# Kernel tuning notes

Hardware: AMD Instinct MI355X
Metric: run time of the kernel (lower is better)

The kernel has to match this reference:

```python
import jax, jax.numpy as jnp
import numpy as np
import math

B, S, D, H = 4, 1024, 1024, 16
DK = D // H
DF = 4 * D
SPARSITY = 0.3
EPS = 1e-5

def _ln(x, g, b):
    mu = jnp.mean(x, axis=-1, keepdims=True)
    var = jnp.mean((x - mu) ** 2, axis=-1, keepdims=True)
    return (x - mu) * jax.lax.rsqrt(var + EPS) * g + b

def setup_inputs() -> dict:
    key = jax.random.key(0)
    ks = jax.random.split(key, 8)
    sc = 0.02
    return {
        "x": jax.random.normal(ks[0], (B, S, D), jnp.float32),
        "Wq": jax.random.normal(ks[1], (D, D), jnp.float32) * sc,
        "bq": jnp.zeros((D,), jnp.float32),
        "Wk": jax.random.normal(ks[2], (D, D), jnp.float32) * sc,
        "bk": jnp.zeros((D,), jnp.float32),
        "Wv": jax.random.normal(ks[3], (D, D), jnp.float32) * sc,
        "bv": jnp.zeros((D,), jnp.float32),
        "Wo": jax.random.normal(ks[4], (D, D), jnp.float32) * sc,
        "bo": jnp.zeros((D,), jnp.float32),
        "W1": jax.random.normal(ks[5], (DF, D), jnp.float32) * sc,
        "b1": jnp.zeros((DF,), jnp.float32),
        "Wm": jax.random.normal(ks[6], (DF, DF), jnp.float32) * sc,
        "bm": jnp.zeros((DF,), jnp.float32),
        "W2": jax.random.normal(ks[7], (D, DF), jnp.float32) * sc,
        "b2": jnp.zeros((D,), jnp.float32),
        "g1": jnp.ones((D,), jnp.float32),
        "be1": jnp.zeros((D,), jnp.float32),
        "g2": jnp.ones((D,), jnp.float32),
        "be2": jnp.zeros((D,), jnp.float32),
    }

def reference(x, Wq, bq, Wk, bk, Wv, bv, Wo, bo, W1, b1, Wm, bm, W2, b2, g1, be1, g2, be2):
    h = _ln(x, g1, be1)
    def heads(W, b):
        return (h @ W.T + b).reshape(B, S, H, DK).transpose(0, 2, 1, 3)  # [B,H,S,DK]
    Q, K, V = heads(Wq, bq), heads(Wk, bk), heads(Wv, bv)
    scores = jnp.einsum("bhqd,bhkd->bhqk", Q, K) / math.sqrt(DK)  # [B,H,S,S]
    k = max(1, int(S * SPARSITY))
    vals, idx = jax.lax.top_k(scores, k)  # [B,H,S,k]
    # scatter top-k values into a -inf canvas (faithful to torch scatter_)
    N = B * H * S
    rows = jnp.arange(N)[:, None]
    mask2 = jnp.full((N, S), -jnp.inf, scores.dtype)
    mask2 = mask2.at[rows, idx.reshape(N, k)].set(vals.reshape(N, k))
    attn = jax.nn.softmax(mask2.reshape(B, H, S, S), axis=-1)
    out = jnp.einsum("bhqk,bhkd->bhqd", attn, V)
    out = out.transpose(0, 2, 1, 3).reshape(B, S, D) @ Wo.T + bo
    x = x + out
    h2 = _ln(x, g2, be2)
    f = jax.nn.gelu(h2 @ W1.T + b1, approximate=False)
    f = jax.nn.gelu(f @ Wm.T + bm, approximate=False)
    f = f @ W2.T + b2
    x = x + f
    return x, attn
```

## Files before the change

### kernel.cpp

```cpp
#include <hip/hip_runtime.h>
#include <hip/hip_bf16.h>

typedef __hip_bfloat16 bf16;
typedef float v4f __attribute__((ext_vector_type(4)));
typedef short v8s __attribute__((ext_vector_type(8)));

#define KSEL 307

__device__ static inline void async16(bf16* lds, const bf16* g) {
    __builtin_amdgcn_global_load_lds(
        (const __attribute__((address_space(1))) void*)g,
        (__attribute__((address_space(3))) void*)lds, 16, 0, 0);
}

__device__ static inline unsigned short f2bu(float f) {
    __hip_bfloat16 h = __float2bfloat16(f);
    return *reinterpret_cast<unsigned short*>(&h);
}

__device__ static inline unsigned pk2(float a, float b) {
    __hip_bfloat162 h = __float22bfloat162_rn(make_float2(a, b));
    return *reinterpret_cast<unsigned*>(&h);
}

__device__ static inline float gelu_f(float v) {
    float c = v * fmaf(v * v, 0.0356774081f, 0.7978845608f);
    return v / (1.0f + __expf(-2.0f * c));
}

struct F2BP { const float* src[7]; bf16* dst[7]; int n4[7]; };

__global__ void __launch_bounds__(256) f2b_multi(F2BP p) {
    int s = blockIdx.y;
    const float* __restrict__ in = p.src[s];
    bf16* __restrict__ out = p.dst[s];
    int n4 = p.n4[s];
    for (int i = blockIdx.x * 256 + threadIdx.x; i < n4; i += gridDim.x * 256) {
        float4 v = ((const float4*)in)[i];
        ushort4 u = make_ushort4(f2bu(v.x), f2bu(v.y), f2bu(v.z), f2bu(v.w));
        ((ushort4*)out)[i] = u;
    }
}

__global__ void __launch_bounds__(256) ln_kernel(const float* __restrict__ x,
                                                 const float* __restrict__ g,
                                                 const float* __restrict__ be,
                                                 bf16* __restrict__ out) {
    int row = blockIdx.x;
    int tid = threadIdx.x;
    const float* xr = x + row * 1024;
    float4 v = ((const float4*)xr)[tid];
    float s = v.x + v.y + v.z + v.w;
    float s2 = v.x*v.x + v.y*v.y + v.z*v.z + v.w*v.w;
    for (int off = 32; off > 0; off >>= 1) {
        s  += __shfl_down(s, off);
        s2 += __shfl_down(s2, off);
    }
    __shared__ float sh[4], sh2[4];
    int w = tid >> 6;
    if ((tid & 63) == 0) { sh[w] = s; sh2[w] = s2; }
    __syncthreads();
    float mean = (sh[0]+sh[1]+sh[2]+sh[3]) * (1.0f / 1024.f);
    float ms   = (sh2[0]+sh2[1]+sh2[2]+sh2[3]) * (1.0f / 1024.f);
    float var  = ms - mean*mean;
    float rs   = rsqrtf(var + 1e-5f);
    float4 gg = ((const float4*)g)[tid];
    float4 bb = ((const float4*)be)[tid];
    ushort4 o = make_ushort4(
        f2bu((v.x-mean)*rs*gg.x + bb.x),
        f2bu((v.y-mean)*rs*gg.y + bb.y),
        f2bu((v.z-mean)*rs*gg.z + bb.z),
        f2bu((v.w-mean)*rs*gg.w + bb.w));
    ((ushort4*)out)[row * 256 + tid] = o;
}

__global__ void __launch_bounds__(256) topk_softmax(unsigned short* __restrict__ scb,
                                                    float* __restrict__ out) {
    __shared__ int hist[4][256];
    const int tid = threadIdx.x;
    const int wid = tid >> 6, lane = tid & 63;
    const long long row = (long long)blockIdx.x * 4 + wid;
    unsigned short* pb = scb + row * 1024;
    float* po = out + row * 1024;
    int* h = hist[wid];

    unsigned short raw[16];
    unsigned key[16];
    float v[16];
#pragma unroll
    for (int j = 0; j < 4; ++j) {
        ushort4 t = *(const ushort4*)(pb + lane * 4 + j * 256);
        raw[j*4+0] = t.x; raw[j*4+1] = t.y; raw[j*4+2] = t.z; raw[j*4+3] = t.w;
    }
#pragma unroll
    for (int j = 0; j < 16; ++j) {
        unsigned u = raw[j];
        key[j] = (u & 0x8000u) ? (0xFFFFu & ~u) : (u | 0x8000u);
        v[j] = __uint_as_float(u << 16);
    }

    unsigned prefix = 0;
    int need = KSEL;
#pragma unroll
    for (int pass = 0; pass < 2; ++pass) {
        const int shift = 8 - 8 * pass;
        *(int4*)&h[lane * 4] = make_int4(0, 0, 0, 0);
        asm volatile("s_waitcnt lgkmcnt(0)" ::: "memory");
#pragma unroll
        for (int j = 0; j < 16; ++j) {
            bool cand = (pass == 0) || ((key[j] >> 8) == prefix);
            if (cand) atomicAdd(&h[(key[j] >> shift) & 255], 1);
        }
        asm volatile("s_waitcnt lgkmcnt(0)" ::: "memory");
        int4 hc = *(const int4*)&h[lane * 4];
        int s_local = hc.x + hc.y + hc.z + hc.w;
        int sfx = s_local;
#pragma unroll
        for (int off = 1; off < 64; off <<= 1) {
            int o = __shfl_down(sfx, off);
            if (lane + off < 64) sfx += o;
        }
        int sfx_next = __shfl_down(sfx, 1);
        if (lane == 63) sfx_next = 0;
        int above_lane = sfx - s_local;
        int suf3 = above_lane + hc.w;
        int suf2 = suf3 + hc.z;
        int suf1 = suf2 + hc.y;
        int suf0 = suf1 + hc.x;
        int bloc = -1, abv = 0;
        if (suf0 >= need && suf1 < need)     { bloc = lane*4+0; abv = suf1; }
        if (suf1 >= need && suf2 < need)     { bloc = lane*4+1; abv = suf2; }
        if (suf2 >= need && suf3 < need)     { bloc = lane*4+2; abv = suf3; }
        if (suf3 >= need && sfx_next < need) { bloc = lane*4+3; abv = sfx_next; }
        unsigned long long mask = __ballot(bloc >= 0);
        int src = __ffsll((unsigned long long)mask) - 1;
        int b = __shfl(bloc, src);
        int above = __shfl(abv, src);
        prefix = (prefix << 8) | (unsigned)b;
        need -= above;
    }

    float mx = v[0];
#pragma unroll
    for (int j = 1; j < 16; ++j) mx = fmaxf(mx, v[j]);
#pragma unroll
    for (int off = 32; off > 0; off >>= 1) mx = fmaxf(mx, __shfl_xor(mx, off));
    float sum = 0.f;
#pragma unroll
    for (int j = 0; j < 16; ++j) {
        bool sel = key[j] >= prefix;
        v[j] = sel ? __expf(v[j] - mx) : 0.f;
        sum += v[j];
    }
#pragma unroll
    for (int off = 32; off > 0; off >>= 1) sum += __shfl_xor(sum, off);
    float inv = 1.0f / sum;
#pragma unroll
    for (int j = 0; j < 4; ++j) {
        float4 o;
        o.x = v[j*4+0]*inv; o.y = v[j*4+1]*inv; o.z = v[j*4+2]*inv; o.w = v[j*4+3]*inv;
        *(float4*)(po + lane * 4 + j * 256) = o;
        uint2 u;
        u.x = pk2(o.x, o.y); u.y = pk2(o.z, o.w);
        *(uint2*)(pb + lane * 4 + j * 256) = u;
    }
}

template<int K, int LDA, int LDB, int LDC, int N, int BMODE, int ACT, int BM>
__global__ void __launch_bounds__(256) gemm_t(const bf16* __restrict__ A,
                                              const bf16* __restrict__ B,
                                              float* __restrict__ Cf,
                                              bf16* __restrict__ Cb,
                                              const float* __restrict__ bias,
                                              const float* __restrict__ resid,
                                              float scale) {
    __shared__ __align__(16) bf16 As[128 * 32];
    __shared__ __align__(16) bf16 Bs[128 * 32];
    int offA = 0, offB = 0, offC = 0;
    if (BM == 1) {
        int z = blockIdx.z;
        int b = z >> 4, h = z & 15;
        offA = b * 1048576 + h * 64;
        offB = offA;
        offC = z * 1048576;
    }
    const int tid = threadIdx.x;
    const int w = tid >> 6, lane = tid & 63;
    const int tm = blockIdx.y * 128, tn = blockIdx.x * 128;
    const int q = lane >> 4, m16 = lane & 15;
    const int r0 = (w >> 1) * 64, c0 = (w & 1) * 64;
    const int srow = lane >> 2;
    const int scol = ((lane & 3) ^ ((lane >> 3) & 3)) * 8;
    const int sq = q ^ ((m16 >> 1) & 3);

    v4f acc[4][4];
#pragma unroll
    for (int i = 0; i < 4; ++i)
#pragma unroll
        for (int j = 0; j < 4; ++j) acc[i][j] = (v4f){0.f, 0.f, 0.f, 0.f};

    const bf16* Ab = A + offA + (tm + w * 16 + srow) * LDA + scol;
    const bf16* Bb = B + offB + (tn + w * 16 + srow) * LDB + scol;
    bf16* Asw = &As[(w * 16) * 32];
    bf16* Bsw = &Bs[(w * 16) * 32];

#pragma unroll 1
    for (int k0 = 0; k0 < K; k0 += 32) {
        async16(Asw,           Ab + k0);
        async16(Asw + 64 * 32, Ab + 64 * LDA + k0);
        async16(Bsw,           Bb + k0);
        async16(Bsw + 64 * 32, Bb + 64 * LDB + k0);
        __syncthreads();
        v8s af[4], bfr[4];
#pragma unroll
        for (int i = 0; i < 4; ++i)
            af[i] = *(const v8s*)&As[(r0 + 16 * i + m16) * 32 + sq * 8];
#pragma unroll
        for (int j = 0; j < 4; ++j)
            bfr[j] = *(const v8s*)&Bs[(c0 + 16 * j + m16) * 32 + sq * 8];
#pragma unroll
        for (int i = 0; i < 4; ++i)
#pragma unroll
            for (int j = 0; j < 4; ++j)
                acc[i][j] = __builtin_amdgcn_mfma_f32_16x16x32_bf16(af[i], bfr[j], acc[i][j], 0, 0, 0);
        __syncthreads();
    }

    float bc[4];
#pragma unroll
    for (int j = 0; j < 4; ++j)
        bc[j] = (BMODE == 1) ? bias[tn + c0 + 16 * j + m16] : 0.f;

#pragma unroll
    for (int i = 0; i < 4; ++i) {
#pragma unroll
        for (int r = 0; r < 4; ++r) {
            int row = tm + r0 + 16 * i + q * 4 + r;
            float br = (BMODE == 2) ? bias[row] : 0.f;
            int rowbase = offC + row * LDC + tn + c0 + m16;
#pragma unroll
            for (int j = 0; j < 4; ++j) {
                float v = acc[i][j][r] * scale + bc[j] + br;
                if (ACT) v = gelu_f(v);
                int idx = rowbase + 16 * j;
                if (resid) v += resid[idx];
                if (Cf) Cf[idx] = v;
                if (Cb) Cb[idx] = __float2bfloat16(v);
            }
        }
    }
}

template<int K, int LDA, int LDB, int LDC, int BMODE>
__global__ void __launch_bounds__(512, 2) gemm128p(const bf16* __restrict__ A,
                                                   const bf16* __restrict__ B,
                                                   float* __restrict__ Cf,
                                                   bf16* __restrict__ Cb,
                                                   const float* __restrict__ bias,
                                                   const float* __restrict__ resid) {
    __shared__ __align__(16) bf16 As[4][128 * 32];
    __shared__ __align__(16) bf16 Bs[4][128 * 32];

    constexpr int nt = K / 32;
    static_assert(nt >= 4, "K >= 128");

    const int tid = threadIdx.x;
    const int w = tid >> 6, lane = tid & 63;
    const int wr = w >> 2, wc = w & 3;
    const int q = lane >> 4, m16 = lane & 15;
    const int tm = blockIdx.y * 128, tn = blockIdx.x * 128;

    const int srow = lane >> 2;
    const int scol = ((lane & 3) ^ ((lane >> 3) & 3)) * 8;
    const bf16* Ag = A + (tm + w * 16 + srow) * LDA + scol;
    const bf16* Bg = B + (tn + w * 16 + srow) * LDB + scol;

    v4f acc[4][2];
#pragma unroll
    for (int i = 0; i < 4; ++i)
#pragma unroll
        for (int j = 0; j < 2; ++j) acc[i][j] = (v4f){0.f, 0.f, 0.f, 0.f};

    const int sq = q ^ ((m16 >> 1) & 3);
    const int aoff = (wr * 64 + m16) * 32 + sq * 8;
    const int boff = (wc * 32 + m16) * 32 + sq * 8;

#pragma unroll
    for (int t = 0; t < 2; ++t) {
        async16(&As[t][(w * 16) * 32], Ag + t * 32);
        async16(&Bs[t][(w * 16) * 32], Bg + t * 32);
    }
    asm volatile("s_waitcnt vmcnt(2)" ::: "memory");
    __builtin_amdgcn_s_barrier();
    __builtin_amdgcn_sched_barrier(0);

#pragma unroll 1
    for (int t = 0; t < nt; ++t) {
        const int cur = t & 3, pre = (t + 2) & 3;
        const int kt = (t + 2 < nt) ? (t + 2) : 0;
        v8s af[4], bfr[2];
#pragma unroll
        for (int i = 0; i < 4; ++i)
            af[i] = *(const v8s*)&As[cur][aoff + i * 512];
#pragma unroll
        for (int j = 0; j < 2; ++j)
            bfr[j] = *(const v8s*)&Bs[cur][boff + j * 512];
        async16(&As[pre][(w * 16) * 32], Ag + kt * 32);
        async16(&Bs[pre][(w * 16) * 32], Bg + kt * 32);
        asm volatile("s_waitcnt lgkmcnt(0)" ::: "memory");
        __builtin_amdgcn_sched_barrier(0);
        __builtin_amdgcn_s_setprio(1);
#pragma unroll
        for (int i = 0; i < 4; ++i)
#pragma unroll
            for (int j = 0; j < 2; ++j)
                acc[i][j] = __builtin_amdgcn_mfma_f32_16x16x32_bf16(af[i], bfr[j], acc[i][j], 0, 0, 0);
        __builtin_amdgcn_s_setprio(0);
        __builtin_amdgcn_sched_barrier(0);
        asm volatile("s_waitcnt vmcnt(2)" ::: "memory");
        __builtin_amdgcn_sched_barrier(0);
        __builtin_amdgcn_s_barrier();
        __builtin_amdgcn_sched_barrier(0);
    }
    asm volatile("s_waitcnt vmcnt(0)" ::: "memory");

    float bc[2];
#pragma unroll
    for (int j = 0; j < 2; ++j)
        bc[j] = (BMODE == 1) ? bias[tn + wc * 32 + 16 * j + m16] : 0.f;

#pragma unroll
    for (int i = 0; i < 4; ++i) {
#pragma unroll
        for (int r = 0; r < 4; ++r) {
            int row = tm + wr * 64 + 16 * i + q * 4 + r;
            float br = (BMODE == 2) ? bias[row] : 0.f;
            int rowbase = row * LDC + tn + wc * 32 + m16;
#pragma unroll
            for (int j = 0; j < 2; ++j) {
                float v = acc[i][j][r] + bc[j] + br;
                int idx = rowbase + 16 * j;
                if (resid) v += resid[idx];
                if (Cf) Cf[idx] = v;
                if (Cb) Cb[idx] = __float2bfloat16(v);
            }
        }
    }
}

template<int K, int LDA, int LDB, int LDC>
__global__ void __launch_bounds__(512, 2) gemm256(const bf16* __restrict__ A,
                                                  const bf16* __restrict__ B,
                                                  bf16* __restrict__ C,
                                                  const float* __restrict__ bias) {
    __shared__ __align__(16) bf16 As[4][256 * 32];
    __shared__ __align__(16) bf16 Bs[4][256 * 32];

    constexpr int nt = K / 32;
    static_assert(nt >= 4 && (nt % 4) == 0, "K must be multiple of 128");

    const int tid = threadIdx.x;
    const int w = tid >> 6, lane = tid & 63;
    const int wm = w >> 2, wn = w & 3;
    const int q = lane >> 4, m16 = lane & 15;

    int bid = blockIdx.y * 16 + blockIdx.x;
    int xcd = bid & 7, inner = bid >> 3;
    int by = (xcd & 3) * 4 + (inner & 3);
    int bx = (xcd >> 2) * 8 + (inner >> 2);
    const int tm = by * 256, tn = bx * 256;

    const int srow = lane >> 2;
    const int scol = ((lane & 3) ^ ((lane >> 3) & 3)) * 8;
    const bf16* Ag = A + (tm + w * 32 + srow) * LDA + scol;
    const bf16* Bg = B + (tn + w * 32 + srow) * LDB + scol;

    v4f acc[8][4];
#pragma unroll
    for (int i = 0; i < 8; ++i)
#pragma unroll
        for (int j = 0; j < 4; ++j) acc[i][j] = (v4f){0.f, 0.f, 0.f, 0.f};

    const int sq = q ^ ((m16 >> 1) & 3);
    const int aoff = (wm * 128 + m16) * 32 + sq * 8;
    const int boff = (wn * 64 + m16) * 32 + sq * 8;

#pragma unroll
    for (int t = 0; t < 2; ++t) {
        async16(&As[t][(w * 32) * 32],      Ag + t * 32);
        async16(&As[t][(w * 32 + 16) * 32], Ag + 16 * LDA + t * 32);
        async16(&Bs[t][(w * 32) * 32],      Bg + t * 32);
        async16(&Bs[t][(w * 32 + 16) * 32], Bg + 16 * LDB + t * 32);
    }
    asm volatile("s_waitcnt vmcnt(4)" ::: "memory");
    __builtin_amdgcn_s_barrier();
    __builtin_amdgcn_sched_barrier(0);

#pragma unroll 1
    for (int t4 = 0; t4 < nt; t4 += 4) {
#pragma unroll
        for (int tt = 0; tt < 4; ++tt) {
            const int t = t4 + tt;
            const int cur = tt;
            const int pre = (tt + 2) & 3;
            int kt = t + 2; if (kt >= nt) kt = 0;
            const bf16* Asrc = Ag + kt * 32;
            const bf16* Bsrc = Bg + kt * 32;

            v8s af[4], bfr[4];
#pragma unroll
            for (int i = 0; i < 4; ++i)
                af[i] = *(const v8s*)&As[cur][aoff + i * 512];
#pragma unroll
            for (int j = 0; j < 4; ++j)
                bfr[j] = *(const v8s*)&Bs[cur][boff + j * 512];
            async16(&As[pre][(w * 32) * 32],      Asrc);
            async16(&As[pre][(w * 32 + 16) * 32], Asrc + 16 * LDA);
            __builtin_amdgcn_s_barrier();
            asm volatile("s_waitcnt lgkmcnt(0)" ::: "memory");
            __builtin_amdgcn_sched_barrier(0);
            __builtin_amdgcn_s_setprio(1);
#pragma unroll
            for (int i = 0; i < 4; ++i)
#pragma unroll
                for (int j = 0; j < 4; ++j)
                    acc[i][j] = __builtin_amdgcn_mfma_f32_16x16x32_bf16(af[i], bfr[j], acc[i][j], 0, 0, 0);
            __builtin_amdgcn_s_setprio(0);
            __builtin_amdgcn_sched_barrier(0);
            __builtin_amdgcn_s_barrier();
            __builtin_amdgcn_sched_barrier(0);

            v8s af2[4];
#pragma unroll
            for (int i = 0; i < 4; ++i)
                af2[i] = *(const v8s*)&As[cur][aoff + 2048 + i * 512];
            async16(&Bs[pre][(w * 32) * 32],      Bsrc);
            async16(&Bs[pre][(w * 32 + 16) * 32], Bsrc + 16 * LDB);
            __builtin_amdgcn_s_barrier();
            asm volatile("s_waitcnt lgkmcnt(0)" ::: "memory");
            __builtin_amdgcn_sched_barrier(0);
            __builtin_amdgcn_s_setprio(1);
#pragma unroll
            for (int i = 0; i < 4; ++i)
#pragma unroll
                for (int j = 0; j < 4; ++j)
                    acc[i + 4][j] = __builtin_amdgcn_mfma_f32_16x16x32_bf16(af2[i], bfr[j], acc[i + 4][j], 0, 0, 0);
            __builtin_amdgcn_s_setprio(0);
            asm volatile("s_waitcnt vmcnt(4)" ::: "memory");
            __builtin_amdgcn_sched_barrier(0);
            __builtin_amdgcn_s_barrier();
            __builtin_amdgcn_sched_barrier(0);
        }
    }

    float bc[4];
#pragma unroll
    for (int j = 0; j < 4; ++j)
        bc[j] = bias[tn + wn * 64 + 16 * j + m16];

#pragma unroll
    for (int i = 0; i < 8; ++i) {
#pragma unroll
        for (int r = 0; r < 4; ++r) {
            int row = tm + wm * 128 + 16 * i + q * 4 + r;
            int rowbase = row * LDC + tn + wn * 64 + m16;
#pragma unroll
            for (int j = 0; j < 4; ++j) {
                float v = acc[i][j][r] + bc[j];
                v = gelu_f(v);
                C[rowbase + 16 * j] = __float2bfloat16(v);
            }
        }
    }
}

__global__ void __launch_bounds__(256) attnv_kernel(const bf16* __restrict__ P,
                                                    const bf16* __restrict__ VT,
                                                    bf16* __restrict__ out) {
    __shared__ __align__(16) bf16 As[4][128 * 32];
    __shared__ __align__(16) bf16 Bs[4][64 * 32];
    int z = blockIdx.z, b = z >> 4, h = z & 15;
    int tid = threadIdx.x, w = tid >> 6, lane = tid & 63;
    int q = lane >> 4, m16 = lane & 15;
    int srow = lane >> 2;
    int scol = ((lane & 3) ^ ((lane >> 3) & 3)) * 8;
    const int sq = q ^ ((m16 >> 1) & 3);

    const bf16* Ab = P + z * 1048576 + (blockIdx.y * 128 + w * 16 + srow) * 1024 + scol;
    const bf16* Bb = VT + (h * 64 + w * 16 + srow) * 4096 + b * 1024 + scol;

    v4f acc[2][4];
#pragma unroll
    for (int i = 0; i < 2; ++i)
#pragma unroll
        for (int j = 0; j < 4; ++j) acc[i][j] = (v4f){0.f, 0.f, 0.f, 0.f};

    const int aoff = (w * 32 + m16) * 32 + sq * 8;
    const int boff = (m16) * 32 + sq * 8;

#pragma unroll
    for (int t = 0; t < 2; ++t) {
        async16(&As[t][(w * 16) * 32],        Ab + t * 32);
        async16(&As[t][(64 + w * 16) * 32],   Ab + 64 * 1024 + t * 32);
        async16(&Bs[t][(w * 16) * 32],        Bb + t * 32);
    }
    asm volatile("s_waitcnt vmcnt(3)" ::: "memory");
    __builtin_amdgcn_s_barrier();
    __builtin_amdgcn_sched_barrier(0);

#pragma unroll 1
    for (int t = 0; t < 32; ++t) {
        const int cur = t & 3, pre = (t + 2) & 3;
        const int kt = (t + 2 < 32) ? (t + 2) : 0;
        v8s af[2], bfr[4];
        af[0] = *(const v8s*)&As[cur][aoff];
        af[1] = *(const v8s*)&As[cur][aoff + 512];
#pragma unroll
        for (int j = 0; j < 4; ++j)
            bfr[j] = *(const v8s*)&Bs[cur][boff + j * 512];
        async16(&As[pre][(w * 16) * 32],      Ab + kt * 32);
        async16(&As[pre][(64 + w * 16) * 32], Ab + 64 * 1024 + kt * 32);
        async16(&Bs[pre][(w * 16) * 32],      Bb + kt * 32);
        asm volatile("s_waitcnt lgkmcnt(0)" ::: "memory");
        __builtin_amdgcn_sched_barrier(0);
        __builtin_amdgcn_s_setprio(1);
#pragma unroll
        for (int i = 0; i < 2; ++i)
#pragma unroll
            for (int j = 0; j < 4; ++j)
                acc[i][j] = __builtin_amdgcn_mfma_f32_16x16x32_bf16(af[i], bfr[j], acc[i][j], 0, 0, 0);
        __builtin_amdgcn_s_setprio(0);
        __builtin_amdgcn_sched_barrier(0);
        asm volatile("s_waitcnt vmcnt(3)" ::: "memory");
        __builtin_amdgcn_sched_barrier(0);
        __builtin_amdgcn_s_barrier();
        __builtin_amdgcn_sched_barrier(0);
    }
    asm volatile("s_waitcnt vmcnt(0)" ::: "memory");

    int orow0 = b * 1024 + blockIdx.y * 128 + w * 32;
#pragma unroll
    for (int i = 0; i < 2; ++i)
#pragma unroll
        for (int r = 0; r < 4; ++r) {
            int row = orow0 + 16 * i + q * 4 + r;
#pragma unroll
            for (int j = 0; j < 4; ++j) {
                int col = h * 64 + 16 * j + m16;
                out[row * 1024 + col] = __float2bfloat16(acc[i][j][r]);
            }
        }
}

extern "C" void kernel_launch(void* const* d_in, const int* in_sizes, int n_in,
                              void* d_out, int out_size, void* d_ws, size_t ws_size,
                              hipStream_t stream) {
    (void)in_sizes; (void)n_in; (void)out_size; (void)ws_size;
    const float* x  = (const float*)d_in[0];
    const float* Wq = (const float*)d_in[1];
    const float* bq = (const float*)d_in[2];
    const float* Wk = (const float*)d_in[3];
    const float* bk = (const float*)d_in[4];
    const float* Wv = (const float*)d_in[5];
    const float* bv = (const float*)d_in[6];
    const float* Wo = (const float*)d_in[7];
    const float* bo = (const float*)d_in[8];
    const float* W1 = (const float*)d_in[9];
    const float* b1 = (const float*)d_in[10];
    const float* Wm = (const float*)d_in[11];
    const float* bm = (const float*)d_in[12];
    const float* W2 = (const float*)d_in[13];
    const float* b2 = (const float*)d_in[14];
    const float* g1 = (const float*)d_in[15];
    const float* be1 = (const float*)d_in[16];
    const float* g2 = (const float*)d_in[17];
    const float* be2 = (const float*)d_in[18];

    char* ws = (char*)d_ws;
    const size_t MB = 1024 * 1024;
    bf16* WQb = (bf16*)(ws + 0 * MB);
    bf16* WKb = (bf16*)(ws + 2 * MB);
    bf16* WVb = (bf16*)(ws + 4 * MB);
    bf16* WOb = (bf16*)(ws + 6 * MB);
    bf16* W1b = (bf16*)(ws + 8 * MB);
    bf16* WMb = (bf16*)(ws + 16 * MB);
    bf16* W2b = (bf16*)(ws + 48 * MB);
    bf16* HB  = (bf16*)(ws + 56 * MB);
    bf16* QB  = (bf16*)(ws + 64 * MB);
    bf16* KB  = (bf16*)(ws + 72 * MB);
    bf16* VT  = (bf16*)(ws + 80 * MB);
    bf16* AT  = (bf16*)(ws + 88 * MB);
    float* X1 = (float*)(ws + 96 * MB);
    bf16* F1  = (bf16*)(ws + 112 * MB);
    bf16* F2  = (bf16*)(ws + 144 * MB);
    bf16* SCb = (bf16*)(ws + 96 * MB);

    float* out_x  = (float*)d_out;
    float* scores = out_x + 4194304;

    F2BP fp;
    fp.src[0] = Wq; fp.dst[0] = WQb; fp.n4[0] = 262144;
    fp.src[1] = Wk; fp.dst[1] = WKb; fp.n4[1] = 262144;
    fp.src[2] = Wv; fp.dst[2] = WVb; fp.n4[2] = 262144;
    fp.src[3] = Wo; fp.dst[3] = WOb; fp.n4[3] = 262144;
    fp.src[4] = W1; fp.dst[4] = W1b; fp.n4[4] = 1048576;
    fp.src[5] = Wm; fp.dst[5] = WMb; fp.n4[5] = 4194304;
    fp.src[6] = W2; fp.dst[6] = W2b; fp.n4[6] = 1048576;
    hipLaunchKernelGGL(f2b_multi, dim3(1024, 7), dim3(256), 0, stream, fp);

    hipLaunchKernelGGL(ln_kernel, dim3(4096), dim3(256), 0, stream, x, g1, be1, HB);

    gemm128p<1024,1024,1024,1024,1><<<dim3(8,32,1), 512, 0, stream>>>(
        HB, WQb, nullptr, QB, bq, nullptr);
    gemm128p<1024,1024,1024,1024,1><<<dim3(8,32,1), 512, 0, stream>>>(
        HB, WKb, nullptr, KB, bk, nullptr);
    gemm128p<1024,1024,1024,4096,2><<<dim3(32,8,1), 512, 0, stream>>>(
        WVb, HB, nullptr, VT, bv, nullptr);

    gemm_t<64,1024,1024,1024,1024,0,0,1><<<dim3(8,8,64), 256, 0, stream>>>(
        QB, KB, nullptr, SCb, nullptr, nullptr, 0.125f);

    hipLaunchKernelGGL(topk_softmax, dim3(16384), dim3(256), 0, stream,
                       (unsigned short*)SCb, scores);

    hipLaunchKernelGGL(attnv_kernel, dim3(1,8,64), dim3(256), 0, stream,
                       SCb, VT, AT);

    gemm128p<1024,1024,1024,1024,1><<<dim3(8,32,1), 512, 0, stream>>>(
        AT, WOb, X1, nullptr, bo, x);

    hipLaunchKernelGGL(ln_kernel, dim3(4096), dim3(256), 0, stream, X1, g2, be2, HB);

    gemm256<1024,1024,1024,4096><<<dim3(16,16,1), 512, 0, stream>>>(HB, W1b, F1, b1);
    gemm256<4096,4096,4096,4096><<<dim3(16,16,1), 512, 0, stream>>>(F1, WMb, F2, bm);

    gemm128p<4096,4096,4096,1024,1><<<dim3(8,32,1), 512, 0, stream>>>(
        F2, W2b, out_x, nullptr, b2, X1);
}
```

Before: 914.1 us.

## Replace radix top-k with ballot bisection, specialize QK kernel, swizzle GEMM blocks

The top-k threshold search drops the two-pass LDS-atomic radix histogram and uses a 16-step binary search over bf16 keys, counting candidates with wave ballots. The QK^T GEMM becomes a dedicated kernel that loads both K=64 slices up front with a single barrier. The 128x128 GEMM gains an XCD-style block-index swizzle and a GELU epilogue option. The first FFN GEMM moves from gemm256 to gemm128p with a 32x32 grid. The trade-off is more ALU/ballot work in top-k in exchange for removing atomics, and changed tile shapes and cache behaviour for the GEMMs.

```diff
diff --git a/kernel.cpp b/kernel.cpp
--- a/kernel.cpp
+++ b/kernel.cpp
@@ -76,69 +76,37 @@
 
 __global__ void __launch_bounds__(256) topk_softmax(unsigned short* __restrict__ scb,
                                                     float* __restrict__ out) {
-    __shared__ int hist[4][256];
     const int tid = threadIdx.x;
     const int wid = tid >> 6, lane = tid & 63;
     const long long row = (long long)blockIdx.x * 4 + wid;
     unsigned short* pb = scb + row * 1024;
     float* po = out + row * 1024;
-    int* h = hist[wid];
-
-    unsigned short raw[16];
+
     unsigned key[16];
     float v[16];
 #pragma unroll
     for (int j = 0; j < 4; ++j) {
         ushort4 t = *(const ushort4*)(pb + lane * 4 + j * 256);
-        raw[j*4+0] = t.x; raw[j*4+1] = t.y; raw[j*4+2] = t.z; raw[j*4+3] = t.w;
+        key[j*4+0] = t.x; key[j*4+1] = t.y; key[j*4+2] = t.z; key[j*4+3] = t.w;
     }
 #pragma unroll
     for (int j = 0; j < 16; ++j) {
-        unsigned u = raw[j];
+        unsigned u = key[j];
+        v[j] = __uint_as_float(u << 16);
         key[j] = (u & 0x8000u) ? (0xFFFFu & ~u) : (u | 0x8000u);
-        v[j] = __uint_as_float(u << 16);
-    }
-
-    unsigned prefix = 0;
-    int need = KSEL;
-#pragma unroll
-    for (int pass = 0; pass < 2; ++pass) {
-        const int shift = 8 - 8 * pass;
-        *(int4*)&h[lane * 4] = make_int4(0, 0, 0, 0);
-        asm volatile("s_waitcnt lgkmcnt(0)" ::: "memory");
-#pragma unroll
-        for (int j = 0; j < 16; ++j) {
-            bool cand = (pass == 0) || ((key[j] >> 8) == prefix);
-            if (cand) atomicAdd(&h[(key[j] >> shift) & 255], 1);
-        }
-        asm volatile("s_waitcnt lgkmcnt(0)" ::: "memory");
-        int4 hc = *(const int4*)&h[lane * 4];
-        int s_local = hc.x + hc.y + hc.z + hc.w;
-        int sfx = s_local;
-#pragma unroll
-        for (int off = 1; off < 64; off <<= 1) {
-            int o = __shfl_down(sfx, off);
-            if (lane + off < 64) sfx += o;
-        }
-        int sfx_next = __shfl_down(sfx, 1);
-        if (lane == 63) sfx_next = 0;
-        int above_lane = sfx - s_local;
-        int suf3 = above_lane + hc.w;
-        int suf2 = suf3 + hc.z;
-        int suf1 = suf2 + hc.y;
-        int suf0 = suf1 + hc.x;
-        int bloc = -1, abv = 0;
-        if (suf0 >= need && suf1 < need)     { bloc = lane*4+0; abv = suf1; }
-        if (suf1 >= need && suf2 < need)     { bloc = lane*4+1; abv = suf2; }
-        if (suf2 >= need && suf3 < need)     { bloc = lane*4+2; abv = suf3; }
-        if (suf3 >= need && sfx_next < need) { bloc = lane*4+3; abv = sfx_next; }
-        unsigned long long mask = __ballot(bloc >= 0);
-        int src = __ffsll((unsigned long long)mask) - 1;
-        int b = __shfl(bloc, src);
-        int above = __shfl(abv, src);
-        prefix = (prefix << 8) | (unsigned)b;
-        need -= above;
-    }
+    }
+
+    unsigned lo = 0, hi = 65536;
+#pragma unroll
+    for (int it = 0; it < 16; ++it) {
+        unsigned mid = (lo + hi) >> 1;
+        int cnt = 0;
+#pragma unroll
+        for (int j = 0; j < 16; ++j)
+            cnt += (int)__popcll(__ballot(key[j] >= mid));
+        if (cnt >= KSEL) lo = mid; else hi = mid;
+    }
+    const unsigned prefix = lo;
 
     float mx = v[0];
 #pragma unroll
@@ -166,24 +134,14 @@
     }
 }
 
-template<int K, int LDA, int LDB, int LDC, int N, int BMODE, int ACT, int BM>
-__global__ void __launch_bounds__(256) gemm_t(const bf16* __restrict__ A,
-                                              const bf16* __restrict__ B,
-                                              float* __restrict__ Cf,
-                                              bf16* __restrict__ Cb,
-                                              const float* __restrict__ bias,
-                                              const float* __restrict__ resid,
-                                              float scale) {
-    __shared__ __align__(16) bf16 As[128 * 32];
-    __shared__ __align__(16) bf16 Bs[128 * 32];
-    int offA = 0, offB = 0, offC = 0;
-    if (BM == 1) {
-        int z = blockIdx.z;
-        int b = z >> 4, h = z & 15;
-        offA = b * 1048576 + h * 64;
-        offB = offA;
-        offC = z * 1048576;
-    }
+__global__ void __launch_bounds__(256) qk_kernel(const bf16* __restrict__ Q,
+                                                 const bf16* __restrict__ Kb,
+                                                 bf16* __restrict__ Cb) {
+    __shared__ __align__(16) bf16 As[2][128 * 32];
+    __shared__ __align__(16) bf16 Bs[2][128 * 32];
+    const int z = blockIdx.z, b = z >> 4, h = z & 15;
+    const int offA = b * 1048576 + h * 64;
+    const int offC = z * 1048576;
     const int tid = threadIdx.x;
     const int w = tid >> 6, lane = tid & 63;
     const int tm = blockIdx.y * 128, tn = blockIdx.x * 128;
@@ -193,65 +151,53 @@
     const int scol = ((lane & 3) ^ ((lane >> 3) & 3)) * 8;
     const int sq = q ^ ((m16 >> 1) & 3);
 
+    const bf16* Ab = Q  + offA + (tm + w * 16 + srow) * 1024 + scol;
+    const bf16* Bb = Kb + offA + (tn + w * 16 + srow) * 1024 + scol;
+
+#pragma unroll
+    for (int s = 0; s < 2; ++s) {
+        async16(&As[s][(w * 16) * 32],       Ab + s * 32);
+        async16(&As[s][(64 + w * 16) * 32],  Ab + 64 * 1024 + s * 32);
+        async16(&Bs[s][(w * 16) * 32],       Bb + s * 32);
+        async16(&Bs[s][(64 + w * 16) * 32],  Bb + 64 * 1024 + s * 32);
+    }
+    __syncthreads();
+
     v4f acc[4][4];
 #pragma unroll
     for (int i = 0; i < 4; ++i)
 #pragma unroll
         for (int j = 0; j < 4; ++j) acc[i][j] = (v4f){0.f, 0.f, 0.f, 0.f};
 
-    const bf16* Ab = A + offA + (tm + w * 16 + srow) * LDA + scol;
-    const bf16* Bb = B + offB + (tn + w * 16 + srow) * LDB + scol;
-    bf16* Asw = &As[(w * 16) * 32];
-    bf16* Bsw = &Bs[(w * 16) * 32];
-
-#pragma unroll 1
-    for (int k0 = 0; k0 < K; k0 += 32) {
-        async16(Asw,           Ab + k0);
-        async16(Asw + 64 * 32, Ab + 64 * LDA + k0);
-        async16(Bsw,           Bb + k0);
-        async16(Bsw + 64 * 32, Bb + 64 * LDB + k0);
-        __syncthreads();
+#pragma unroll
+    for (int s = 0; s < 2; ++s) {
         v8s af[4], bfr[4];
 #pragma unroll
         for (int i = 0; i < 4; ++i)
-            af[i] = *(const v8s*)&As[(r0 + 16 * i + m16) * 32 + sq * 8];
+            af[i] = *(const v8s*)&As[s][(r0 + 16 * i + m16) * 32 + sq * 8];
 #pragma unroll
         for (int j = 0; j < 4; ++j)
-            bfr[j] = *(const v8s*)&Bs[(c0 + 16 * j + m16) * 32 + sq * 8];
+            bfr[j] = *(const v8s*)&Bs[s][(c0 + 16 * j + m16) * 32 + sq * 8];
 #pragma unroll
         for (int i = 0; i < 4; ++i)
 #pragma unroll
             for (int j = 0; j < 4; ++j)
                 acc[i][j] = __builtin_amdgcn_mfma_f32_16x16x32_bf16(af[i], bfr[j], acc[i][j], 0, 0, 0);
-        __syncthreads();
-    }
-
-    float bc[4];
-#pragma unroll
-    for (int j = 0; j < 4; ++j)
-        bc[j] = (BMODE == 1) ? bias[tn + c0 + 16 * j + m16] : 0.f;
-
-#pragma unroll
-    for (int i = 0; i < 4; ++i) {
+    }
+
+#pragma unroll
+    for (int i = 0; i < 4; ++i)
 #pragma unroll
         for (int r = 0; r < 4; ++r) {
             int row = tm + r0 + 16 * i + q * 4 + r;
-            float br = (BMODE == 2) ? bias[row] : 0.f;
-            int rowbase = offC + row * LDC + tn + c0 + m16;
-#pragma unroll
-            for (int j = 0; j < 4; ++j) {
-                float v = acc[i][j][r] * scale + bc[j] + br;
-                if (ACT) v = gelu_f(v);
-                int idx = rowbase + 16 * j;
-                if (resid) v += resid[idx];
-                if (Cf) Cf[idx] = v;
-                if (Cb) Cb[idx] = __float2bfloat16(v);
-            }
+            int rowbase = offC + row * 1024 + tn + c0 + m16;
+#pragma unroll
+            for (int j = 0; j < 4; ++j)
+                Cb[rowbase + 16 * j] = __float2bfloat16(acc[i][j][r] * 0.125f);
         }
-    }
-}
-
-template<int K, int LDA, int LDB, int LDC, int BMODE>
+}
+
+template<int K, int LDA, int LDB, int LDC, int BMODE, int ACT, int SWZ>
 __global__ void __launch_bounds__(512, 2) gemm128p(const bf16* __restrict__ A,
                                                    const bf16* __restrict__ B,
                                                    float* __restrict__ Cf,
@@ -268,7 +214,16 @@
     const int w = tid >> 6, lane = tid & 63;
     const int wr = w >> 2, wc = w & 3;
     const int q = lane >> 4, m16 = lane & 15;
-    const int tm = blockIdx.y * 128, tn = blockIdx.x * 128;
+
+    int bx = blockIdx.x, by = blockIdx.y;
+    if (SWZ) {
+        int nx = gridDim.x;
+        int bid = by * nx + bx;
+        int nwg = nx * gridDim.y;
+        int nb = (bid & 7) * (nwg >> 3) + (bid >> 3);
+        bx = nb % nx; by = nb / nx;
+    }
+    const int tm = by * 128, tn = bx * 128;
 
     const int srow = lane >> 2;
     const int scol = ((lane & 3) ^ ((lane >> 3) & 3)) * 8;
@@ -339,6 +294,7 @@
 #pragma unroll
             for (int j = 0; j < 2; ++j) {
                 float v = acc[i][j][r] + bc[j] + br;
+                if (ACT) v = gelu_f(v);
                 int idx = rowbase + 16 * j;
                 if (resid) v += resid[idx];
                 if (Cf) Cf[idx] = v;
@@ -610,15 +566,14 @@
 
     hipLaunchKernelGGL(ln_kernel, dim3(4096), dim3(256), 0, stream, x, g1, be1, HB);
 
-    gemm128p<1024,1024,1024,1024,1><<<dim3(8,32,1), 512, 0, stream>>>(
+    gemm128p<1024,1024,1024,1024,1,0,1><<<dim3(8,32,1), 512, 0, stream>>>(
         HB, WQb, nullptr, QB, bq, nullptr);
-    gemm128p<1024,1024,1024,1024,1><<<dim3(8,32,1), 512, 0, stream>>>(
+    gemm128p<1024,1024,1024,1024,1,0,1><<<dim3(8,32,1), 512, 0, stream>>>(
         HB, WKb, nullptr, KB, bk, nullptr);
-    gemm128p<1024,1024,1024,4096,2><<<dim3(32,8,1), 512, 0, stream>>>(
+    gemm128p<1024,1024,1024,4096,2,0,1><<<dim3(32,8,1), 512, 0, stream>>>(
         WVb, HB, nullptr, VT, bv, nullptr);
 
-    gemm_t<64,1024,1024,1024,1024,0,0,1><<<dim3(8,8,64), 256, 0, stream>>>(
-        QB, KB, nullptr, SCb, nullptr, nullptr, 0.125f);
+    hipLaunchKernelGGL(qk_kernel, dim3(8,8,64), dim3(256), 0, stream, QB, KB, SCb);
 
     hipLaunchKernelGGL(topk_softmax, dim3(16384), dim3(256), 0, stream,
                        (unsigned short*)SCb, scores);
@@ -626,14 +581,15 @@
     hipLaunchKernelGGL(attnv_kernel, dim3(1,8,64), dim3(256), 0, stream,
                        SCb, VT, AT);
 
-    gemm128p<1024,1024,1024,1024,1><<<dim3(8,32,1), 512, 0, stream>>>(
+    gemm128p<1024,1024,1024,1024,1,0,1><<<dim3(8,32,1), 512, 0, stream>>>(
         AT, WOb, X1, nullptr, bo, x);
 
     hipLaunchKernelGGL(ln_kernel, dim3(4096), dim3(256), 0, stream, X1, g2, be2, HB);
 
-    gemm256<1024,1024,1024,4096><<<dim3(16,16,1), 512, 0, stream>>>(HB, W1b, F1, b1);
+    gemm128p<1024,1024,1024,4096,1,1,1><<<dim3(32,32,1), 512, 0, stream>>>(
+        HB, W1b, nullptr, F1, b1, nullptr);
     gemm256<4096,4096,4096,4096><<<dim3(16,16,1), 512, 0, stream>>>(F1, WMb, F2, bm);
 
-    gemm128p<4096,4096,4096,1024,1><<<dim3(8,32,1), 512, 0, stream>>>(
+    gemm128p<4096,4096,4096,1024,1,0,1><<<dim3(8,32,1), 512, 0, stream>>>(
         F2, W2b, out_x, nullptr, b2, X1);
 }
```

After: 897.9 us. Within noise of the previous version (-1.8%).
